# Optimization experiments

Hardware: AMD Instinct MI355X
Metric: run time of the kernel (lower is better)

The kernel has to match this reference:

```python
import jax, jax.numpy as jnp
import numpy as np

D_MODEL = 1024
NUM_HEADS = 16
D_K = D_MODEL // NUM_HEADS
SCALE = D_K ** -0.5
NEG = -1e9


def _split_heads(t):
    B, L, D = t.shape
    return t.reshape(B, L, NUM_HEADS, D_K).transpose(0, 2, 1, 3)  # (B,H,L,dk)


def _tropical_scores(Q, K):
    # max over d_k of Q[...,i,d] + K[...,j,d] without materializing (B,H,L,L,dk)
    Qd = jnp.moveaxis(Q, -1, 0)  # (dk,B,H,L)
    Kd = jnp.moveaxis(K, -1, 0)
    B, H, L, _ = Q.shape
    init = jnp.full((B, H, L, L), -jnp.inf, Q.dtype)
    def step(carry, qk):
        q, k = qk  # (B,H,L) each
        return jnp.maximum(carry, q[..., :, None] + k[..., None, :]), None
    out, _ = jax.lax.scan(step, init, (Qd, Kd))
    return out


def setup_inputs() -> dict:
    key = jax.random.key(0)
    ks = jax.random.split(key, 10)
    B, L = 2, 1024
    x = jax.random.normal(ks[0], (B, L, D_MODEL), dtype=jnp.float32)
    # causal mask (B,1,L,L)
    mask = jnp.broadcast_to(jnp.tril(jnp.ones((L, L), dtype=bool)), (B, 1, L, L))
    s = 0.02
    Wq = jax.random.normal(ks[1], (D_MODEL, D_MODEL), jnp.float32) * s
    Wk = jax.random.normal(ks[2], (D_MODEL, D_MODEL), jnp.float32) * s
    Wv = jax.random.normal(ks[3], (D_MODEL, D_MODEL), jnp.float32) * s
    Wo = jax.random.normal(ks[4], (D_MODEL, D_MODEL), jnp.float32) * s
    bq = jnp.zeros((D_MODEL,), jnp.float32)
    bk = jnp.zeros((D_MODEL,), jnp.float32)
    bv = jnp.zeros((D_MODEL,), jnp.float32)
    bo = jnp.zeros((D_MODEL,), jnp.float32)
    # score_gate: weight zero-init, bias = -2.0 (as in torch module)
    Wg = jnp.zeros((NUM_HEADS, D_MODEL), jnp.float32)
    bg = jnp.full((NUM_HEADS,), -2.0, jnp.float32)
    # log temperatures, init_temp=1.0 -> log(1)=0
    log_temps = jnp.zeros((NUM_HEADS,), jnp.float32)
    return {"x": x, "mask": mask, "Wq": Wq, "bq": bq, "Wk": Wk, "bk": bk,
            "Wv": Wv, "bv": bv, "Wo": Wo, "bo": bo, "Wg": Wg, "bg": bg,
            "log_temps": log_temps}


def reference(x, mask, Wq, bq, Wk, bk, Wv, bv, Wo, bo, Wg, bg, log_temps):
    B, L, D = x.shape
    Q = _split_heads(x @ Wq.T + bq)
    K = _split_heads(x @ Wk.T + bk)
    V = _split_heads(x @ Wv.T + bv)
    class_scores = jnp.einsum('bhqd,bhkd->bhqk', Q, K) * SCALE
    trop_scores = _tropical_scores(Q, K) * SCALE
    # per-query, per-head gate g in (0,1): (B,L,H) -> (B,H,L,1)
    g = jax.nn.sigmoid(x @ Wg.T + bg).transpose(0, 2, 1)[..., None]
    scores = g * trop_scores + (1.0 - g) * class_scores
    scores = jnp.where(mask, scores, NEG)
    tau = jnp.clip(jnp.exp(log_temps), 0.02, 10.0).reshape(1, NUM_HEADS, 1, 1)
    attn = jax.nn.softmax(scores / tau, axis=-1)
    out = jnp.einsum('bhqk,bhkd->bhqd', attn, V)
    out = out.transpose(0, 2, 1, 3).reshape(B, L, D)
    return out @ Wo.T + bo, attn
```

## Files before the change

### kernel.cpp

```cpp
#include <hip/hip_runtime.h>


typedef _Float16 f16;
typedef __attribute__((ext_vector_type(2))) _Float16 h2;
typedef __attribute__((ext_vector_type(8))) _Float16 f16x8;
typedef __attribute__((ext_vector_type(4))) float f32x4;

__device__ inline f32x4 mfma_f16(f16x8 a, f16x8 b, f32x4 c) {
    return __builtin_amdgcn_mfma_f32_16x16x32_f16(a, b, c, 0, 0, 0);
}

__device__ inline void async_copy16(const f16* g, f16* l) {
    __builtin_amdgcn_global_load_lds((const __attribute__((address_space(1))) void*)g,
                                     (__attribute__((address_space(3))) void*)l, 16, 0, 0);
}

__device__ inline float dot2acc(h2 a, h2 b, float c) {
#if __has_builtin(__builtin_amdgcn_fdot2)
    return __builtin_amdgcn_fdot2(a, b, c, false);
#else
    c = fmaf((float)a[0], (float)b[0], c);
    return fmaf((float)a[1], (float)b[1], c);
#endif
}

__global__ __launch_bounds__(256) void cvt_all(const float* __restrict__ x,
                                               const float* __restrict__ Wq,
                                               const float* __restrict__ Wk,
                                               const float* __restrict__ Wv,
                                               const float* __restrict__ Wo,
                                               const float* __restrict__ Wg,
                                               f16* __restrict__ x16,
                                               f16* __restrict__ w16,
                                               f16* __restrict__ wo16) {
    int i = blockIdx.x * 256 + threadIdx.x;
    if (i >= 1576960) {
        int off = i - 1576960;
        *(uint2*)(w16 + (size_t)(3088 << 10) + (size_t)off * 4) = make_uint2(0u, 0u);
        return;
    }
    const float* s;
    f16* d;
    int off;
    if (i < 524288)       { s = x;  d = x16;                        off = i; }
    else if (i < 786432)  { s = Wq; d = w16;                        off = i - 524288; }
    else if (i < 1048576) { s = Wk; d = w16 + (1 << 20);            off = i - 786432; }
    else if (i < 1310720) { s = Wv; d = w16 + (2 << 20);            off = i - 1048576; }
    else if (i < 1572864) { s = Wo; d = wo16;                       off = i - 1310720; }
    else                  { s = Wg; d = w16 + (size_t)(3072 << 10); off = i - 1572864; }
    float4 v = *(const float4*)(s + (size_t)off * 4);
    f16 o[4] = {(f16)v.x, (f16)v.y, (f16)v.z, (f16)v.w};
    *(uint2*)(d + (size_t)off * 4) = *(uint2*)o;
}

template <bool OUT16, bool VTR, bool GATE>
__global__ __launch_bounds__(256) void gemm128(const f16* __restrict__ A,
                                               const f16* __restrict__ B,
                                               void* __restrict__ Cv,
                                               const float* __restrict__ b0,
                                               const float* __restrict__ b1,
                                               const float* __restrict__ b2,
                                               const float* __restrict__ bgv,
                                               f16* __restrict__ vt,
                                               float* __restrict__ gbuf,
                                               int K, int lda, int ldb, int ldc) {
    __shared__ f16 At[128 * 32];
    __shared__ f16 Bt[64 * 32];
    const int t = threadIdx.x;
    const int m0 = blockIdx.y * 128, n0 = blockIdx.x * 64;
    const int wave = t >> 6, lane = t & 63;
    const int l16 = lane & 15, quad = lane >> 4;
    const int wm = (wave >> 1) * 64, wn = (wave & 1) * 32;
    const int sr = t >> 2, sc = (t & 3) * 8;
    f32x4 acc[4][2] = {};
    for (int k0 = 0; k0 < K; k0 += 32) {
        __syncthreads();
#pragma unroll
        for (int i = 0; i < 2; ++i)
            async_copy16(A + (size_t)(m0 + sr + i * 64) * lda + k0 + sc, &At[t * 8 + i * 2048]);
        async_copy16(B + (size_t)(n0 + sr) * ldb + k0 + sc, &Bt[t * 8]);
        __syncthreads();
        f16x8 af[4], bfr[2];
#pragma unroll
        for (int i = 0; i < 4; ++i)
            af[i] = *(const f16x8*)&At[(wm + i * 16 + l16) * 32 + quad * 8];
#pragma unroll
        for (int i = 0; i < 2; ++i)
            bfr[i] = *(const f16x8*)&Bt[(wn + i * 16 + l16) * 32 + quad * 8];
#pragma unroll
        for (int mi = 0; mi < 4; ++mi)
#pragma unroll
            for (int ni = 0; ni < 2; ++ni)
                acc[mi][ni] = mfma_f16(af[mi], bfr[ni], acc[mi][ni]);
    }
#pragma unroll
    for (int mi = 0; mi < 4; ++mi) {
#pragma unroll
        for (int ni = 0; ni < 2; ++ni) {
            int gcol = n0 + wn + ni * 16 + l16;
            if (GATE && n0 >= 3072) {
                int hd = gcol - 3072;
                if (hd < 16) {
                    float bias = bgv[hd];
#pragma unroll
                    for (int rg = 0; rg < 4; ++rg) {
                        int grow = m0 + wm + mi * 16 + quad * 4 + rg;
                        float v = acc[mi][ni][rg] + bias;
                        gbuf[(size_t)grow * 16 + hd] = 1.0f / (1.0f + __expf(-v));
                    }
                }
            } else if (VTR && n0 >= 2048) {
                const float* bp = b2;
                float bias = bp[gcol & 1023];
                int hd = gcol - 2048;
                int h = hd >> 6, d = hd & 63;
                int k0r = m0 + wm + mi * 16 + quad * 4;
                int b = k0r >> 10;
                f16 o4[4];
#pragma unroll
                for (int rg = 0; rg < 4; ++rg) o4[rg] = (f16)(acc[mi][ni][rg] + bias);
                *(uint2*)&vt[((size_t)((b * 16 + h) * 64 + d)) * 1024 + (k0r & 1023)] =
                    *(uint2*)o4;
            } else {
                const float* bp = (gcol < 1024) ? b0 : (gcol < 2048 ? b1 : b2);
                float bias = bp[gcol & 1023];
#pragma unroll
                for (int rg = 0; rg < 4; ++rg) {
                    int grow = m0 + wm + mi * 16 + quad * 4 + rg;
                    float v = acc[mi][ni][rg] + bias;
                    if (OUT16)
                        ((f16*)Cv)[(size_t)grow * ldc + gcol] = (f16)v;
                    else
                        ((float*)Cv)[(size_t)grow * ldc + gcol] = v;
                }
            }
        }
    }
}

__global__ __launch_bounds__(256) void scores_fused(const f16* __restrict__ qkv16,
                                                    const f16* __restrict__ vt16,
                                                    const float* __restrict__ gbuf,
                                                    const float* __restrict__ log_temps,
                                                    float* __restrict__ attn,
                                                    f16* __restrict__ oh) {
    __shared__ f16 Qs[16][64];
    __shared__ f16 Ssm[16][1032];
    __shared__ float gsm[16];
    const int t = threadIdx.x;
    const int qt = 63 - (blockIdx.x >> 5);
    const int bh = blockIdx.x & 31;
    const int b = bh & 1, h = bh >> 1;
    const int q0 = qt << 4;
    {
        int rr = t >> 4, cc = (t & 15) * 4;
        *(uint2*)&Qs[rr][cc] =
            *(const uint2*)(qkv16 + (size_t)(b * 1024 + q0 + rr) * 3072 + h * 64 + cc);
    }
    if (t < 16) gsm[t] = gbuf[(size_t)(b * 1024 + q0 + t) * 16 + h];
    float tau = __expf(log_temps[h]);
    tau = fminf(fmaxf(tau, 0.02f), 10.0f);
    const float invtau = 1.0f / tau;
    __syncthreads();

    const int qmax = q0 + 15;
    const int npass = (qmax >> 9) + 1;
    for (int p = 0; p < npass; ++p) {
        const int k1 = (p << 9) + t;
        const int k2 = k1 + 256;
        const bool a1 = (k1 <= qmax), a2 = (k2 <= qmax);
        if (a1) {
            const f16* Kp1 = qkv16 + (size_t)(b * 1024 + k1) * 3072 + 1024 + h * 64;
            h2 kr1[32], kr2[32];
#pragma unroll
            for (int i = 0; i < 8; ++i) *(f16x8*)&kr1[i * 4] = ((const f16x8*)Kp1)[i];
            if (a2) {
                const f16* Kp2 = qkv16 + (size_t)(b * 1024 + k2) * 3072 + 1024 + h * 64;
#pragma unroll
                for (int i = 0; i < 8; ++i) *(f16x8*)&kr2[i * 4] = ((const f16x8*)Kp2)[i];
            }
#pragma unroll 2
            for (int q = 0; q < 16; ++q) {
                h2 qr[32];
#pragma unroll
                for (int i = 0; i < 8; ++i) *(f16x8*)&qr[i * 4] = *(const f16x8*)&Qs[q][i * 8];
                float g = gsm[q];
                {
                    float dot = 0.f;
                    h2 tm2 = {(f16)-65504.f, (f16)-65504.f};
#pragma unroll
                    for (int i = 0; i < 32; ++i) {
                        h2 qa = qr[i];
                        h2 s2 = qa + kr1[i];
                        tm2 = __builtin_elementwise_max(tm2, s2);
                        dot = dot2acc(qa, kr1[i], dot);
                    }
                    float tm = fmaxf((float)tm2[0], (float)tm2[1]);
                    Ssm[q][k1] = (f16)((g * tm + (1.0f - g) * dot) * 0.125f);
                }
                if (a2) {
                    float dot = 0.f;
                    h2 tm2 = {(f16)-65504.f, (f16)-65504.f};
#pragma unroll
                    for (int i = 0; i < 32; ++i) {
                        h2 qa = qr[i];
                        h2 s2 = qa + kr2[i];
                        tm2 = __builtin_elementwise_max(tm2, s2);
                        dot = dot2acc(qa, kr2[i], dot);
                    }
                    float tm = fmaxf((float)tm2[0], (float)tm2[1]);
                    Ssm[q][k2] = (f16)((g * tm + (1.0f - g) * dot) * 0.125f);
                }
            }
        }
    }
    __syncthreads();

    const int lane = t & 63, w = t >> 6;
    const int l16 = lane & 15, quad = lane >> 4;
#pragma unroll
    for (int j = 0; j < 4; ++j) {
        int q = w * 4 + j;
        int qg = q0 + q;
        float m = -1e30f;
        for (int k = lane; k <= qg; k += 64) m = fmaxf(m, (float)Ssm[q][k]);
#pragma unroll
        for (int o = 32; o > 0; o >>= 1) m = fmaxf(m, __shfl_xor(m, o));
        float ssum = 0.f;
        for (int k = lane; k <= qg; k += 64) {
            float e = __expf(((float)Ssm[q][k] - m) * invtau);
            Ssm[q][k] = (f16)e;
            ssum += e;
        }
#pragma unroll
        for (int o = 32; o > 0; o >>= 1) ssum += __shfl_xor(ssum, o);
        float inv = 1.0f / ssum;
        float* orow = attn + ((size_t)((b * 16 + h) * 1024 + qg) << 10);
        for (int k = lane; k < 1024; k += 64) {
            float val = (k <= qg) ? (float)Ssm[q][k] * inv : 0.0f;
            orow[k] = val;
            Ssm[q][k] = (f16)val;
        }
    }
    __syncthreads();

    {
        const int dw = w * 16;
        f32x4 acc = {};
        const int nkt = (q0 + 47) >> 5;
        const f16* Vb = vt16 + ((size_t)((b * 16 + h) * 64 + dw + l16)) * 1024 + quad * 8;
#pragma unroll 4
        for (int kt = 0; kt < nkt; ++kt) {
            const int kb = kt << 5;
            f16x8 a = *(const f16x8*)&Ssm[l16][kb + quad * 8];
            f16x8 bf = *(const f16x8*)(Vb + kb);
            acc = mfma_f16(a, bf, acc);
        }
#pragma unroll
        for (int rg = 0; rg < 4; ++rg)
            oh[(size_t)(b * 1024 + q0 + quad * 4 + rg) * 1024 + h * 64 + dw + l16] =
                (f16)acc[rg];
    }
}

extern "C" void kernel_launch(void* const* d_in, const int* in_sizes, int n_in,
                              void* d_out, int out_size, void* d_ws, size_t ws_size,
                              hipStream_t stream) {
    const float* x  = (const float*)d_in[0];
    const float* Wq = (const float*)d_in[2];
    const float* bq = (const float*)d_in[3];
    const float* Wk = (const float*)d_in[4];
    const float* bk = (const float*)d_in[5];
    const float* Wv = (const float*)d_in[6];
    const float* bv = (const float*)d_in[7];
    const float* Wo = (const float*)d_in[8];
    const float* bo = (const float*)d_in[9];
    const float* Wg = (const float*)d_in[10];
    const float* bg = (const float*)d_in[11];
    const float* lt = (const float*)d_in[12];
    float* out = (float*)d_out;
    float* attn = out + (size_t)2 * 1024 * 1024;

    char* ws = (char*)d_ws;
    const size_t KB = (size_t)1 << 10;
    f16*   x16   = (f16*)ws;
    f16*   w16   = (f16*)(ws + 4096 * KB);
    f16*   wo16  = (f16*)(ws + 10368 * KB);
    f16*   qkv16 = (f16*)(ws + 12416 * KB);
    f16*   vt16  = (f16*)(ws + 24704 * KB);
    float* gbuf  = (float*)(ws + 28800 * KB);
    f16*   oh16  = (f16*)(ws + 28928 * KB);

    cvt_all<<<6208, 256, 0, stream>>>(x, Wq, Wk, Wv, Wo, Wg, x16, w16, wo16);
    gemm128<true, true, true><<<dim3(49, 16), 256, 0, stream>>>(
        x16, w16, qkv16, bq, bk, bv, bg, vt16, gbuf, 1024, 1024, 1024, 3072);
    scores_fused<<<2048, 256, 0, stream>>>(qkv16, vt16, gbuf, lt, attn, oh16);
    gemm128<false, false, false><<<dim3(16, 16), 256, 0, stream>>>(
        oh16, wo16, out, bo, bo, bo, nullptr, nullptr, nullptr, 1024, 1024, 1024, 1024);
}
```

Before: 298.9 us.

## Register-block four keys per thread in fused tropical/classic score loop

Each thread now handles four consecutive keys held in registers instead of two keys spaced 256 apart. Every Q row loaded from LDS is therefore reused across four keys, and the four max and dot accumulator chains are split in two to add instruction-level parallelism. Results go to LDS as one packed 8-byte store, and the kernel is pinned to two waves per EU with an asm barrier so the K registers stay resident. The cost is much higher register pressure, lower occupancy, and causal load imbalance when query tiles are short, since only threads with k0 <= qmax do work.

After: 351.8 us. +17.7%, slower.

```diff
diff --git a/kernel.cpp b/kernel.cpp
--- a/kernel.cpp
+++ b/kernel.cpp
@@ -5,6 +5,7 @@
 typedef __attribute__((ext_vector_type(2))) _Float16 h2;
 typedef __attribute__((ext_vector_type(8))) _Float16 f16x8;
 typedef __attribute__((ext_vector_type(4))) float f32x4;
+typedef __attribute__((ext_vector_type(4))) unsigned int u32x4;
 
 __device__ inline f32x4 mfma_f16(f16x8 a, f16x8 b, f32x4 c) {
     return __builtin_amdgcn_mfma_f32_16x16x32_f16(a, b, c, 0, 0, 0);
@@ -138,12 +139,13 @@
     }
 }
 
-__global__ __launch_bounds__(256) void scores_fused(const f16* __restrict__ qkv16,
-                                                    const f16* __restrict__ vt16,
-                                                    const float* __restrict__ gbuf,
-                                                    const float* __restrict__ log_temps,
-                                                    float* __restrict__ attn,
-                                                    f16* __restrict__ oh) {
+__global__ __launch_bounds__(256) __attribute__((amdgpu_waves_per_eu(2, 2)))
+void scores_fused(const f16* __restrict__ qkv16,
+                  const f16* __restrict__ vt16,
+                  const float* __restrict__ gbuf,
+                  const float* __restrict__ log_temps,
+                  float* __restrict__ attn,
+                  f16* __restrict__ oh) {
     __shared__ f16 Qs[16][64];
     __shared__ f16 Ssm[16][1032];
     __shared__ float gsm[16];
@@ -164,53 +166,81 @@
     __syncthreads();
 
     const int qmax = q0 + 15;
-    const int npass = (qmax >> 9) + 1;
-    for (int p = 0; p < npass; ++p) {
-        const int k1 = (p << 9) + t;
-        const int k2 = k1 + 256;
-        const bool a1 = (k1 <= qmax), a2 = (k2 <= qmax);
-        if (a1) {
-            const f16* Kp1 = qkv16 + (size_t)(b * 1024 + k1) * 3072 + 1024 + h * 64;
-            h2 kr1[32], kr2[32];
-#pragma unroll
-            for (int i = 0; i < 8; ++i) *(f16x8*)&kr1[i * 4] = ((const f16x8*)Kp1)[i];
-            if (a2) {
-                const f16* Kp2 = qkv16 + (size_t)(b * 1024 + k2) * 3072 + 1024 + h * 64;
-#pragma unroll
-                for (int i = 0; i < 8; ++i) *(f16x8*)&kr2[i * 4] = ((const f16x8*)Kp2)[i];
+
+    {
+        const int k0 = t * 4;
+        if (k0 <= qmax) {
+            h2 kr0[32], kr1[32], kr2[32], kr3[32];
+            const f16* Kp = qkv16 + (size_t)(b * 1024 + k0) * 3072 + 1024 + h * 64;
+#pragma unroll
+            for (int i = 0; i < 8; ++i) {
+                *(f16x8*)&kr0[i * 4] = *(const f16x8*)(Kp + i * 8);
+                *(f16x8*)&kr1[i * 4] = *(const f16x8*)(Kp + 3072 + i * 8);
+                *(f16x8*)&kr2[i * 4] = *(const f16x8*)(Kp + 6144 + i * 8);
+                *(f16x8*)&kr3[i * 4] = *(const f16x8*)(Kp + 9216 + i * 8);
             }
-#pragma unroll 2
+#pragma unroll
+            for (int j = 0; j < 8; ++j) {
+                asm volatile("" : "+v"(*(u32x4*)&kr0[j * 4]), "+v"(*(u32x4*)&kr1[j * 4]),
+                                  "+v"(*(u32x4*)&kr2[j * 4]), "+v"(*(u32x4*)&kr3[j * 4]));
+            }
             for (int q = 0; q < 16; ++q) {
                 h2 qr[32];
 #pragma unroll
-                for (int i = 0; i < 8; ++i) *(f16x8*)&qr[i * 4] = *(const f16x8*)&Qs[q][i * 8];
-                float g = gsm[q];
+                for (int i = 0; i < 8; ++i)
+                    *(f16x8*)&qr[i * 4] = *(const f16x8*)&Qs[q][i * 8];
+                const float g = gsm[q];
+                const float gi = 1.0f - g;
+                h2 ma0 = qr[0] + kr0[0], mb0 = qr[1] + kr0[1];
+                h2 ma1 = qr[0] + kr1[0], mb1 = qr[1] + kr1[1];
+                h2 ma2 = qr[0] + kr2[0], mb2 = qr[1] + kr2[1];
+                h2 ma3 = qr[0] + kr3[0], mb3 = qr[1] + kr3[1];
+                float da0 = dot2acc(qr[0], kr0[0], 0.f), db0 = dot2acc(qr[1], kr0[1], 0.f);
+                float da1 = dot2acc(qr[0], kr1[0], 0.f), db1 = dot2acc(qr[1], kr1[1], 0.f);
+                float da2 = dot2acc(qr[0], kr2[0], 0.f), db2 = dot2acc(qr[1], kr2[1], 0.f);
+                float da3 = dot2acc(qr[0], kr3[0], 0.f), db3 = dot2acc(qr[1], kr3[1], 0.f);
+#pragma unroll
+                for (int i = 2; i < 32; i += 2) {
+                    h2 qa = qr[i], qb = qr[i + 1];
+                    ma0 = __builtin_elementwise_max(ma0, qa + kr0[i]);
+                    mb0 = __builtin_elementwise_max(mb0, qb + kr0[i + 1]);
+                    da0 = dot2acc(qa, kr0[i], da0);
+                    db0 = dot2acc(qb, kr0[i + 1], db0);
+                    ma1 = __builtin_elementwise_max(ma1, qa + kr1[i]);
+                    mb1 = __builtin_elementwise_max(mb1, qb + kr1[i + 1]);
+                    da1 = dot2acc(qa, kr1[i], da1);
+                    db1 = dot2acc(qb, kr1[i + 1], db1);
+                    ma2 = __builtin_elementwise_max(ma2, qa + kr2[i]);
+                    mb2 = __builtin_elementwise_max(mb2, qb + kr2[i + 1]);
+                    da2 = dot2acc(qa, kr2[i], da2);
+                    db2 = dot2acc(qb, kr2[i + 1], db2);
+                    ma3 = __builtin_elementwise_max(ma3, qa + kr3[i]);
+                    mb3 = __builtin_elementwise_max(mb3, qb + kr3[i + 1]);
+                    da3 = dot2acc(qa, kr3[i], da3);
+                    db3 = dot2acc(qb, kr3[i + 1], db3);
+                }
+                f16 o4[4];
                 {
-                    float dot = 0.f;
-                    h2 tm2 = {(f16)-65504.f, (f16)-65504.f};
-#pragma unroll
-                    for (int i = 0; i < 32; ++i) {
-                        h2 qa = qr[i];
-                        h2 s2 = qa + kr1[i];
-                        tm2 = __builtin_elementwise_max(tm2, s2);
-                        dot = dot2acc(qa, kr1[i], dot);
-                    }
-                    float tm = fmaxf((float)tm2[0], (float)tm2[1]);
-                    Ssm[q][k1] = (f16)((g * tm + (1.0f - g) * dot) * 0.125f);
-                }
-                if (a2) {
-                    float dot = 0.f;
-                    h2 tm2 = {(f16)-65504.f, (f16)-65504.f};
-#pragma unroll
-                    for (int i = 0; i < 32; ++i) {
-                        h2 qa = qr[i];
-                        h2 s2 = qa + kr2[i];
-                        tm2 = __builtin_elementwise_max(tm2, s2);
-                        dot = dot2acc(qa, kr2[i], dot);
-                    }
-                    float tm = fmaxf((float)tm2[0], (float)tm2[1]);
-                    Ssm[q][k2] = (f16)((g * tm + (1.0f - g) * dot) * 0.125f);
-                }
+                    h2 tc = __builtin_elementwise_max(ma0, mb0);
+                    float tm = fmaxf((float)tc[0], (float)tc[1]);
+                    o4[0] = (f16)((g * tm + gi * (da0 + db0)) * 0.125f);
+                }
+                {
+                    h2 tc = __builtin_elementwise_max(ma1, mb1);
+                    float tm = fmaxf((float)tc[0], (float)tc[1]);
+                    o4[1] = (f16)((g * tm + gi * (da1 + db1)) * 0.125f);
+                }
+                {
+                    h2 tc = __builtin_elementwise_max(ma2, mb2);
+                    float tm = fmaxf((float)tc[0], (float)tc[1]);
+                    o4[2] = (f16)((g * tm + gi * (da2 + db2)) * 0.125f);
+                }
+                {
+                    h2 tc = __builtin_elementwise_max(ma3, mb3);
+                    float tm = fmaxf((float)tc[0], (float)tc[1]);
+                    o4[3] = (f16)((g * tm + gi * (da3 + db3)) * 0.125f);
+                }
+                *(uint2*)&Ssm[q][k0] = *(uint2*)o4;
             }
         }
     }
```

## Compute classical QK dot products with MFMA before the tropical max pass

Applied to the files above, without the earlier changes.

Moves the classical Q·K dot product out of the per-thread scalar fdot2 loop and into a separate MFMA pass that writes fp16 dot scores into shared memory. The tropical max loop then reads these dots back and only does packed add/max, now split into two independent max chains for more instruction-level parallelism. Costs an extra LDS round trip and barrier, stores the dot rounded to fp16 before combining, and pads the Q tile in shared memory.

Result: no change. 303.3 us (+1.5%).

```diff
diff --git a/kernel.cpp b/kernel.cpp
--- a/kernel.cpp
+++ b/kernel.cpp
@@ -13,15 +13,6 @@
 __device__ inline void async_copy16(const f16* g, f16* l) {
     __builtin_amdgcn_global_load_lds((const __attribute__((address_space(1))) void*)g,
                                      (__attribute__((address_space(3))) void*)l, 16, 0, 0);
-}
-
-__device__ inline float dot2acc(h2 a, h2 b, float c) {
-#if __has_builtin(__builtin_amdgcn_fdot2)
-    return __builtin_amdgcn_fdot2(a, b, c, false);
-#else
-    c = fmaf((float)a[0], (float)b[0], c);
-    return fmaf((float)a[1], (float)b[1], c);
-#endif
 }
 
 __global__ __launch_bounds__(256) void cvt_all(const float* __restrict__ x,
@@ -144,7 +135,7 @@
                                                     const float* __restrict__ log_temps,
                                                     float* __restrict__ attn,
                                                     f16* __restrict__ oh) {
-    __shared__ f16 Qs[16][64];
+    __shared__ f16 Qs[16][80];
     __shared__ f16 Ssm[16][1032];
     __shared__ float gsm[16];
     const int t = threadIdx.x;
@@ -152,6 +143,8 @@
     const int bh = blockIdx.x & 31;
     const int b = bh & 1, h = bh >> 1;
     const int q0 = qt << 4;
+    const int lane = t & 63, w = t >> 6;
+    const int l16 = lane & 15, quad = lane >> 4;
     {
         int rr = t >> 4, cc = (t & 15) * 4;
         *(uint2*)&Qs[rr][cc] =
@@ -164,60 +157,78 @@
     __syncthreads();
 
     const int qmax = q0 + 15;
-    const int npass = (qmax >> 9) + 1;
-    for (int p = 0; p < npass; ++p) {
-        const int k1 = (p << 9) + t;
-        const int k2 = k1 + 256;
-        const bool a1 = (k1 <= qmax), a2 = (k2 <= qmax);
-        if (a1) {
-            const f16* Kp1 = qkv16 + (size_t)(b * 1024 + k1) * 3072 + 1024 + h * 64;
-            h2 kr1[32], kr2[32];
-#pragma unroll
-            for (int i = 0; i < 8; ++i) *(f16x8*)&kr1[i * 4] = ((const f16x8*)Kp1)[i];
-            if (a2) {
-                const f16* Kp2 = qkv16 + (size_t)(b * 1024 + k2) * 3072 + 1024 + h * 64;
-#pragma unroll
-                for (int i = 0; i < 8; ++i) *(f16x8*)&kr2[i * 4] = ((const f16x8*)Kp2)[i];
-            }
+
+    {
+        f16x8 qf0 = *(const f16x8*)&Qs[l16][quad * 8];
+        f16x8 qf1 = *(const f16x8*)&Qs[l16][32 + quad * 8];
+        const f16* Kb = qkv16 + (size_t)(b * 1024 + l16) * 3072 + 1024 + h * 64 + quad * 8;
+        for (int kb = w * 16; kb <= qmax; kb += 64) {
+            f16x8 kf0 = *(const f16x8*)(Kb + (size_t)kb * 3072);
+            f16x8 kf1 = *(const f16x8*)(Kb + (size_t)kb * 3072 + 32);
+            f32x4 acc = {};
+            acc = mfma_f16(kf0, qf0, acc);
+            acc = mfma_f16(kf1, qf1, acc);
+            f16 o4[4];
+#pragma unroll
+            for (int rg = 0; rg < 4; ++rg) o4[rg] = (f16)acc[rg];
+            *(uint2*)&Ssm[l16][kb + quad * 4] = *(uint2*)o4;
+        }
+    }
+    __syncthreads();
+
+    {
+        const int npass = (qmax >> 9) + 1;
+        for (int p = 0; p < npass; ++p) {
+            const int k1 = (p << 9) + t;
+            const int k2 = k1 + 256;
+            const bool a1 = (k1 <= qmax), a2 = (k2 <= qmax);
+            if (a1) {
+                const f16* Kp1 = qkv16 + (size_t)(b * 1024 + k1) * 3072 + 1024 + h * 64;
+                h2 kr1[32], kr2[32];
+#pragma unroll
+                for (int i = 0; i < 8; ++i) *(f16x8*)&kr1[i * 4] = ((const f16x8*)Kp1)[i];
+                if (a2) {
+                    const f16* Kp2 = qkv16 + (size_t)(b * 1024 + k2) * 3072 + 1024 + h * 64;
+#pragma unroll
+                    for (int i = 0; i < 8; ++i) *(f16x8*)&kr2[i * 4] = ((const f16x8*)Kp2)[i];
+                }
 #pragma unroll 2
-            for (int q = 0; q < 16; ++q) {
-                h2 qr[32];
-#pragma unroll
-                for (int i = 0; i < 8; ++i) *(f16x8*)&qr[i * 4] = *(const f16x8*)&Qs[q][i * 8];
-                float g = gsm[q];
-                {
-                    float dot = 0.f;
-                    h2 tm2 = {(f16)-65504.f, (f16)-65504.f};
-#pragma unroll
-                    for (int i = 0; i < 32; ++i) {
-                        h2 qa = qr[i];
-                        h2 s2 = qa + kr1[i];
-                        tm2 = __builtin_elementwise_max(tm2, s2);
-                        dot = dot2acc(qa, kr1[i], dot);
+                for (int q = 0; q < 16; ++q) {
+                    h2 qr[32];
+#pragma unroll
+                    for (int i = 0; i < 8; ++i)
+                        *(f16x8*)&qr[i * 4] = *(const f16x8*)&Qs[q][i * 8];
+                    const float g = gsm[q];
+                    {
+                        float dot = (float)Ssm[q][k1];
+                        h2 ta = qr[0] + kr1[0], tb = qr[1] + kr1[1];
+#pragma unroll
+                        for (int i = 2; i < 32; i += 2) {
+                            ta = __builtin_elementwise_max(ta, qr[i] + kr1[i]);
+                            tb = __builtin_elementwise_max(tb, qr[i + 1] + kr1[i + 1]);
+                        }
+                        h2 tc = __builtin_elementwise_max(ta, tb);
+                        float tm = fmaxf((float)tc[0], (float)tc[1]);
+                        Ssm[q][k1] = (f16)((g * tm + (1.0f - g) * dot) * 0.125f);
                     }
-                    float tm = fmaxf((float)tm2[0], (float)tm2[1]);
-                    Ssm[q][k1] = (f16)((g * tm + (1.0f - g) * dot) * 0.125f);
-                }
-                if (a2) {
-                    float dot = 0.f;
-                    h2 tm2 = {(f16)-65504.f, (f16)-65504.f};
-#pragma unroll
-                    for (int i = 0; i < 32; ++i) {
-                        h2 qa = qr[i];
-                        h2 s2 = qa + kr2[i];
-                        tm2 = __builtin_elementwise_max(tm2, s2);
-                        dot = dot2acc(qa, kr2[i], dot);
+                    if (a2) {
+                        float dot = (float)Ssm[q][k2];
+                        h2 ta = qr[0] + kr2[0], tb = qr[1] + kr2[1];
+#pragma unroll
+                        for (int i = 2; i < 32; i += 2) {
+                            ta = __builtin_elementwise_max(ta, qr[i] + kr2[i]);
+                            tb = __builtin_elementwise_max(tb, qr[i + 1] + kr2[i + 1]);
+                        }
+                        h2 tc = __builtin_elementwise_max(ta, tb);
+                        float tm = fmaxf((float)tc[0], (float)tc[1]);
+                        Ssm[q][k2] = (f16)((g * tm + (1.0f - g) * dot) * 0.125f);
                     }
-                    float tm = fmaxf((float)tm2[0], (float)tm2[1]);
-                    Ssm[q][k2] = (f16)((g * tm + (1.0f - g) * dot) * 0.125f);
                 }
             }
         }
     }
     __syncthreads();
 
-    const int lane = t & 63, w = t >> 6;
-    const int l16 = lane & 15, quad = lane >> 4;
 #pragma unroll
     for (int j = 0; j < 4; ++j) {
         int q = w * 4 + j;
```
